# Optimization experiments

Hardware: AMD Instinct MI355X
Metric: run time of the kernel (lower is better)

## Reference

```python
import jax, jax.numpy as jnp
import numpy as np

D_MODEL = 1024
ED = 2048        # d_inner = expand_factor * d_model
N = 16           # d_state
DT_RANK = 64     # ceil(d_model/16)
K = 4            # d_conv
B_SZ = 4
L = 512


def _causal_depthwise_conv(u, w, b):
    # u: [B, L, ED], w: [ED, 1, K], b: [ED]
    xc = jnp.transpose(u, (0, 2, 1))  # [B, ED, L]
    xc = jax.lax.conv_general_dilated(
        xc, w, window_strides=(1,), padding=[(K - 1, 0)],
        feature_group_count=ED, dimension_numbers=('NCH', 'OIH', 'NCH'))
    xc = xc + b[None, :, None]
    return jnp.transpose(xc, (0, 2, 1))  # [B, L, ED]


def _ssm_branch(xz_half, z, conv_w, conv_b, Wx, Wdt, b_dt, A_log, Dp):
    # xz_half, z: [B, L, ED]
    x = jax.nn.silu(_causal_depthwise_conv(xz_half, conv_w, conv_b))
    dbc = x @ Wx.T  # [B, L, dt_rank + 2N]
    delta = dbc[..., :DT_RANK]
    Bm = dbc[..., DT_RANK:DT_RANK + N]
    Cm = dbc[..., DT_RANK + N:]
    delta = jax.nn.softplus(delta @ Wdt.T + b_dt)  # [B, L, ED]
    A = -jnp.exp(A_log)  # [ED, N]
    dA = jnp.exp(delta[..., None] * A)                        # [B, L, ED, N]
    bx = (delta[..., None] * Bm[:, :, None, :]) * x[..., None]  # [B, L, ED, N]
    dA_t = jnp.transpose(dA, (1, 0, 2, 3))
    bx_t = jnp.transpose(bx, (1, 0, 2, 3))
    c_t = jnp.transpose(Cm, (1, 0, 2))  # [L, B, N]
    h0 = jnp.zeros((x.shape[0], ED, N), dtype=x.dtype)

    def step(h, inp):
        dAi, bxi, ci = inp
        h = dAi * h + bxi
        return h, jnp.einsum('ben,bn->be', h, ci)

    _, ys = jax.lax.scan(step, h0, (dA_t, bx_t, c_t))
    y = jnp.transpose(ys, (1, 0, 2)) + Dp * x  # D skip connection
    return y * jax.nn.silu(z)                  # gate


def _mamba_block(x, W_in, conv_w, conv_b, Wx, Wdt, b_dt, A_log, Dp,
                 conv_w_b, conv_b_b, Wx_b, Wdt_b, b_dt_b, A_log_b, Dp_b, W_out):
    xz = x @ W_in.T  # [B, L, 2*ED]
    xf, zf = xz[..., :ED], xz[..., ED:]
    y = _ssm_branch(xf, zf, conv_w, conv_b, Wx, Wdt, b_dt, A_log, Dp)
    xz_r = xz[:, ::-1, :]
    xb, zb = xz_r[..., :ED], xz_r[..., ED:]
    y_b = _ssm_branch(xb, zb, conv_w_b, conv_b_b, Wx_b, Wdt_b, b_dt_b, A_log_b, Dp_b)
    y = (y + y_b[:, ::-1, :]) * 0.5
    return y @ W_out.T


def setup_inputs() -> dict:
    key = jax.random.key(0)
    ks = jax.random.split(key, 20)
    s = lambda k, shp, sc: jax.random.normal(k, shp, dtype=jnp.float32) * sc
    dt = jnp.exp(jax.random.uniform(ks[15], (ED,)) * (np.log(0.1) - np.log(0.001)) + np.log(0.001))
    dt = jnp.clip(dt, 1e-4, None)
    inv_dt = dt + jnp.log(-jnp.expm1(-dt))
    A_init = jnp.log(jnp.tile(jnp.arange(1, N + 1, dtype=jnp.float32), (ED, 1)))
    return {
        'x': s(ks[0], (B_SZ, L, D_MODEL), 1.0),
        'W_in': s(ks[1], (2 * ED, D_MODEL), D_MODEL ** -0.5),
        'conv_w': s(ks[2], (ED, 1, K), K ** -0.5),
        'conv_b': s(ks[3], (ED,), 0.02),
        'Wx': s(ks[4], (DT_RANK + 2 * N, ED), ED ** -0.5),
        'Wdt': jax.random.uniform(ks[5], (ED, DT_RANK), minval=-DT_RANK ** -0.5, maxval=DT_RANK ** -0.5),
        'b_dt': inv_dt,
        'A_log': A_init,
        'Dp': jnp.ones((ED,), dtype=jnp.float32),
        'conv_w_b': s(ks[6], (ED, 1, K), K ** -0.5),
        'conv_b_b': s(ks[7], (ED,), 0.02),
        'Wx_b': s(ks[8], (DT_RANK + 2 * N, ED), ED ** -0.5),
        'Wdt_b': jax.random.uniform(ks[9], (ED, DT_RANK), minval=-DT_RANK ** -0.5, maxval=DT_RANK ** -0.5),
        'b_dt_b': inv_dt,
        'A_log_b': A_init,
        'Dp_b': jnp.ones((ED,), dtype=jnp.float32),
        'W_out': s(ks[10], (D_MODEL, ED), ED ** -0.5),
    }


def reference(x, W_in, conv_w, conv_b, Wx, Wdt, b_dt, A_log, Dp,
              conv_w_b, conv_b_b, Wx_b, Wdt_b, b_dt_b, A_log_b, Dp_b, W_out):
    return _mamba_block(x, W_in, conv_w, conv_b, Wx, Wdt, b_dt, A_log, Dp,
                        conv_w_b, conv_b_b, Wx_b, Wdt_b, b_dt_b, A_log_b, Dp_b, W_out)
```

## Files before the change

### kernel.cpp

```cpp
#include <hip/hip_runtime.h>
#include <hip/hip_bf16.h>
#include <stdint.h>

typedef unsigned short ushort_t;
typedef __attribute__((ext_vector_type(8))) short short8;
typedef __attribute__((ext_vector_type(4))) float f32x4;
typedef __attribute__((ext_vector_type(2))) float f32x2;

__device__ __forceinline__ float b2f(ushort_t u) {
    union { uint32_t i; float f; } v; v.i = ((uint32_t)u) << 16; return v.f;
}
__device__ __forceinline__ ushort_t f2b(float f) {
    union { float f; uint32_t i; } v; v.f = f;
    uint32_t r = v.i + 0x7fff + ((v.i >> 16) & 1);
    return (ushort_t)(r >> 16);
}

#if __has_builtin(__builtin_amdgcn_exp2f)
#define EXP2(x) __builtin_amdgcn_exp2f(x)
#else
#define EXP2(x) __expf((x) * 0.69314718056f)
#endif

__device__ __forceinline__ void ll16(const ushort_t* g, ushort_t* l) {
    __builtin_amdgcn_global_load_lds(
        (const __attribute__((address_space(1))) uint32_t*)g,
        (__attribute__((address_space(3))) uint32_t*)l, 16, 0, 0);
}

template <int CTRL>
__device__ __forceinline__ float dpp_add(float p) {
    int v = __builtin_amdgcn_update_dpp(0, __float_as_int(p), CTRL, 0xF, 0xF, true);
    return p + __int_as_float(v);
}
#define DPP_XOR1 0xB1
#define DPP_XOR2 0x4E
#define DPP_HMIR 0x141

__device__ __forceinline__ void epi_wave_f32(
    float* sw, const f32x4* accg, float* dst0, int ldc, int lane)
{
    const int quad = lane >> 4, lr = lane & 15;
#pragma unroll
    for (int j = 0; j < 4; j++)
#pragma unroll
        for (int r = 0; r < 4; r++)
            sw[(quad * 4 + r) * 64 + j * 16 + lr] = accg[j][r];
    __asm__ volatile("s_waitcnt lgkmcnt(0)" ::: "memory");
#pragma unroll
    for (int t = 0; t < 4; t++) {
        int row = t * 4 + quad;
        float4 v = *(const float4*)(&sw[row * 64 + lr * 4]);
        *(float4*)(dst0 + (size_t)row * ldc + lr * 4) = v;
    }
}

__device__ __forceinline__ void epi_wave_b16(
    float* sw, const f32x4* accg, ushort_t* dst0, int ldc, int lane)
{
    const int quad = lane >> 4, lr = lane & 15;
#pragma unroll
    for (int j = 0; j < 4; j++)
#pragma unroll
        for (int r = 0; r < 4; r++)
            sw[(quad * 4 + r) * 64 + j * 16 + lr] = accg[j][r];
    __asm__ volatile("s_waitcnt lgkmcnt(0)" ::: "memory");
#pragma unroll
    for (int t = 0; t < 4; t++) {
        int row = t * 4 + quad;
        float4 v = *(const float4*)(&sw[row * 64 + lr * 4]);
        ushort4 o; o.x = f2b(v.x); o.y = f2b(v.y); o.z = f2b(v.z); o.w = f2b(v.w);
        *(ushort4*)(dst0 + (size_t)row * ldc + lr * 4) = o;
    }
}

struct CastSeg { const float4* src; ushort4* dst; };
struct CastArgs { CastSeg seg[7]; int start[8]; };

__global__ __launch_bounds__(256) void cast_multi(CastArgs a)
{
    int g = blockIdx.x * 256 + threadIdx.x;
    if (g >= a.start[7]) return;
    int s = 0;
#pragma unroll
    for (int i = 1; i < 7; i++) s += (g >= a.start[i]);
    int i = g - a.start[s];
    float4 v = a.seg[s].src[i];
    ushort4 o;
    o.x = f2b(v.x); o.y = f2b(v.y); o.z = f2b(v.z); o.w = f2b(v.w);
    a.seg[s].dst[i] = o;
}

#define BK 32

__global__ __launch_bounds__(256) void gemm_g1(
    const ushort_t* __restrict__ A, int lda,
    const ushort_t* __restrict__ B, int ldb,
    ushort_t* __restrict__ Cout, int ldc, int Kd)
{
    __shared__ ushort_t As[2][128 * BK];
    __shared__ ushort_t Bs[2][128 * BK];
    __shared__ float sepi[4][1024];

    const int tid  = threadIdx.x;
    const int m0   = blockIdx.y * 128;
    const int n0   = blockIdx.x * 128;
    const int wv   = tid >> 6;
    const int lane = tid & 63;
    const int wm   = (wv >> 1) * 64;
    const int wn   = (wv & 1) * 64;
    const int lr   = lane & 15;
    const int quad = lane >> 4;

    f32x4 acc[4][4];
#pragma unroll
    for (int i = 0; i < 4; i++)
#pragma unroll
        for (int j = 0; j < 4; j++) acc[i][j] = f32x4{0.f, 0.f, 0.f, 0.f};

    const int srA = wv * 32 + (lane >> 2);
    const int scA = (lane & 3) * 8;

    auto stage = [&](int bf_, int k0) {
        ll16(A + (size_t)(m0 + srA) * lda + k0 + scA,      &As[bf_][wv * 1024]);
        ll16(A + (size_t)(m0 + srA + 16) * lda + k0 + scA, &As[bf_][wv * 1024 + 512]);
        ll16(B + (size_t)(n0 + srA) * ldb + k0 + scA,      &Bs[bf_][wv * 1024]);
        ll16(B + (size_t)(n0 + srA + 16) * ldb + k0 + scA, &Bs[bf_][wv * 1024 + 512]);
    };

    const int nk = Kd / BK;
    stage(0, 0);
    __syncthreads();

    for (int t = 0; t < nk; ++t) {
        const int buf = t & 1;
        if (t + 1 < nk) stage(buf ^ 1, (t + 1) * BK);

        short8 af[4], bfr[4];
#pragma unroll
        for (int i = 0; i < 4; i++)
            af[i] = *(const short8*)(&As[buf][(wm + i * 16 + lr) * BK + quad * 8]);
#pragma unroll
        for (int j = 0; j < 4; j++)
            bfr[j] = *(const short8*)(&Bs[buf][(wn + j * 16 + lr) * BK + quad * 8]);
#pragma unroll
        for (int i = 0; i < 4; i++)
#pragma unroll
            for (int j = 0; j < 4; j++)
                acc[i][j] = __builtin_amdgcn_mfma_f32_16x16x32_bf16(af[i], bfr[j], acc[i][j], 0, 0, 0);
        __syncthreads();
    }

#pragma unroll
    for (int g = 0; g < 4; g++)
        epi_wave_b16(sepi[wv], acc[g],
                     Cout + (size_t)(m0 + wm + g * 16) * ldc + n0 + wn, ldc, lane);
}

__global__ __launch_bounds__(256) void gemm_g4(
    const ushort_t* __restrict__ A, int lda,
    const ushort_t* __restrict__ B, int ldb,
    float* __restrict__ Cout, int ldc, int Kd)
{
    __shared__ ushort_t As[2][64 * BK];
    __shared__ ushort_t Bs[2][128 * BK];
    __shared__ float sepi[4][1024];

    const int tid  = threadIdx.x;
    const int m0   = blockIdx.y * 64;
    const int n0   = blockIdx.x * 128;
    const int wv   = tid >> 6;
    const int lane = tid & 63;
    const int wm   = (wv >> 1) * 32;
    const int wn   = (wv & 1) * 64;
    const int lr   = lane & 15;
    const int quad = lane >> 4;

    f32x4 acc[2][4];
#pragma unroll
    for (int i = 0; i < 2; i++)
#pragma unroll
        for (int j = 0; j < 4; j++) acc[i][j] = f32x4{0.f, 0.f, 0.f, 0.f};

    const int srA = wv * 16 + (lane >> 2);
    const int srB = wv * 32 + (lane >> 2);
    const int sc  = (lane & 3) * 8;

    auto stage = [&](int bf_, int k0) {
        ll16(A + (size_t)(m0 + srA) * lda + k0 + sc,      &As[bf_][wv * 512]);
        ll16(B + (size_t)(n0 + srB) * ldb + k0 + sc,      &Bs[bf_][wv * 1024]);
        ll16(B + (size_t)(n0 + srB + 16) * ldb + k0 + sc, &Bs[bf_][wv * 1024 + 512]);
    };

    const int nk = Kd / BK;
    stage(0, 0);
    __syncthreads();

    for (int t = 0; t < nk; ++t) {
        const int buf = t & 1;
        if (t + 1 < nk) stage(buf ^ 1, (t + 1) * BK);

        short8 af[2], bfr[4];
#pragma unroll
        for (int i = 0; i < 2; i++)
            af[i] = *(const short8*)(&As[buf][(wm + i * 16 + lr) * BK + quad * 8]);
#pragma unroll
        for (int j = 0; j < 4; j++)
            bfr[j] = *(const short8*)(&Bs[buf][(wn + j * 16 + lr) * BK + quad * 8]);
#pragma unroll
        for (int i = 0; i < 2; i++)
#pragma unroll
            for (int j = 0; j < 4; j++)
                acc[i][j] = __builtin_amdgcn_mfma_f32_16x16x32_bf16(af[i], bfr[j], acc[i][j], 0, 0, 0);
        __syncthreads();
    }

#pragma unroll
    for (int g = 0; g < 2; g++)
        epi_wave_f32(sepi[wv], acc[g],
                     Cout + (size_t)(m0 + wm + g * 16) * ldc + n0 + wn, ldc, lane);
}

__global__ __launch_bounds__(256) void gemm_g2(
    const ushort_t* __restrict__ xc, const ushort_t* __restrict__ wx,
    float* __restrict__ part)
{
    __shared__ ushort_t As[2][128 * BK];
    __shared__ ushort_t Bs[2][128 * BK];
    __shared__ float sepi[4][1024];

    const int sk = blockIdx.x, mb = blockIdx.y, br = blockIdx.z;
    const ushort_t* A = xc + (size_t)br * 2048 * 2048;
    const ushort_t* B = wx + (size_t)br * 96 * 2048;
    float* C = part + (size_t)(sk * 2 + br) * 2048 * 96;
    const int m0 = mb * 128;
    const int kb = sk * 256;

    const int tid  = threadIdx.x;
    const int wv   = tid >> 6;
    const int lane = tid & 63;
    const int wm   = (wv >> 1) * 64;
    const int wn   = (wv & 1) * 64;
    const int lr   = lane & 15;
    const int quad = lane >> 4;

    f32x4 acc[4][4];
#pragma unroll
    for (int i = 0; i < 4; i++)
#pragma unroll
        for (int j = 0; j < 4; j++) acc[i][j] = f32x4{0.f, 0.f, 0.f, 0.f};

    const int srA = wv * 32 + (lane >> 2);
    const int sc  = (lane & 3) * 8;

    auto stage = [&](int bf_, int k0) {
        ll16(A + (size_t)(m0 + srA) * 2048 + k0 + sc,      &As[bf_][wv * 1024]);
        ll16(A + (size_t)(m0 + srA + 16) * 2048 + k0 + sc, &As[bf_][wv * 1024 + 512]);
        ll16(B + (size_t)(srA) * 2048 + k0 + sc,           &Bs[bf_][wv * 1024]);
        ll16(B + (size_t)(srA + 16) * 2048 + k0 + sc,      &Bs[bf_][wv * 1024 + 512]);
    };

    stage(0, kb);
    __syncthreads();

    for (int t = 0; t < 8; ++t) {
        const int buf = t & 1;
        if (t + 1 < 8) stage(buf ^ 1, kb + (t + 1) * BK);

        short8 af[4], bfr[4];
#pragma unroll
        for (int i = 0; i < 4; i++)
            af[i] = *(const short8*)(&As[buf][(wm + i * 16 + lr) * BK + quad * 8]);
#pragma unroll
        for (int j = 0; j < 4; j++)
            bfr[j] = *(const short8*)(&Bs[buf][(wn + j * 16 + lr) * BK + quad * 8]);
#pragma unroll
        for (int i = 0; i < 4; i++)
#pragma unroll
            for (int j = 0; j < 4; j++)
                acc[i][j] = __builtin_amdgcn_mfma_f32_16x16x32_bf16(af[i], bfr[j], acc[i][j], 0, 0, 0);
        __syncthreads();
    }

    float* sw = sepi[wv];
#pragma unroll
    for (int g = 0; g < 4; g++) {
#pragma unroll
        for (int j = 0; j < 4; j++)
#pragma unroll
            for (int r = 0; r < 4; r++)
                sw[(quad * 4 + r) * 64 + j * 16 + lr] = acc[g][j][r];
        __asm__ volatile("s_waitcnt lgkmcnt(0)" ::: "memory");
        int col = wn + lr * 4;
#pragma unroll
        for (int t = 0; t < 4; t++) {
            int row = t * 4 + quad;
            if (col < 96) {
                float4 v = *(const float4*)(&sw[row * 64 + lr * 4]);
                *(float4*)(C + (size_t)(m0 + wm + g * 16 + row) * 96 + col) = v;
            }
        }
    }
}

__global__ __launch_bounds__(256) void reduce_dbc(
    const float4* __restrict__ part, ushort4* __restrict__ dbc16)
{
    int g = blockIdx.x * 256 + threadIdx.x;
    const int S = 2 * 2048 * 96 / 4;
    float4 r = part[g];
#pragma unroll
    for (int i = 1; i < 8; i++) {
        float4 p = part[g + i * S];
        r.x += p.x; r.y += p.y; r.z += p.z; r.w += p.w;
    }
    ushort4 o; o.x = f2b(r.x); o.y = f2b(r.y); o.z = f2b(r.z); o.w = f2b(r.w);
    dbc16[g] = o;
}

__global__ __launch_bounds__(256) void gemm_g3(
    const ushort_t* __restrict__ dbc16, const ushort_t* __restrict__ wdt,
    ushort_t* __restrict__ delta,
    const float* __restrict__ bdt_f, const float* __restrict__ bdt_b)
{
    __shared__ ushort_t As[2][128 * BK];
    __shared__ ushort_t Bs[2][128 * BK];
    __shared__ float sepi[4][1024];

    const int br = blockIdx.z;
    const ushort_t* A = dbc16 + (size_t)br * 2048 * 96;
    const ushort_t* B = wdt + (size_t)br * 2048 * 64;
    ushort_t* C = delta + (size_t)br * 2048 * 2048;
    const float* bias = br ? bdt_b : bdt_f;

    const int tid  = threadIdx.x;
    const int m0   = blockIdx.y * 128;
    const int n0   = blockIdx.x * 128;
    const int wv   = tid >> 6;
    const int lane = tid & 63;
    const int wm   = (wv >> 1) * 64;
    const int wn   = (wv & 1) * 64;
    const int lr   = lane & 15;
    const int quad = lane >> 4;

    f32x4 acc[4][4];
#pragma unroll
    for (int i = 0; i < 4; i++)
#pragma unroll
        for (int j = 0; j < 4; j++) acc[i][j] = f32x4{0.f, 0.f, 0.f, 0.f};

    const int srA = wv * 32 + (lane >> 2);
    const int sc  = (lane & 3) * 8;

    auto stage = [&](int bf_, int k0) {
        ll16(A + (size_t)(m0 + srA) * 96 + k0 + sc,       &As[bf_][wv * 1024]);
        ll16(A + (size_t)(m0 + srA + 16) * 96 + k0 + sc,  &As[bf_][wv * 1024 + 512]);
        ll16(B + (size_t)(n0 + srA) * 64 + k0 + sc,       &Bs[bf_][wv * 1024]);
        ll16(B + (size_t)(n0 + srA + 16) * 64 + k0 + sc,  &Bs[bf_][wv * 1024 + 512]);
    };

    stage(0, 0);
    __syncthreads();

    for (int t = 0; t < 2; ++t) {
        const int buf = t & 1;
        if (t + 1 < 2) stage(buf ^ 1, (t + 1) * BK);

        short8 af[4], bfr[4];
#pragma unroll
        for (int i = 0; i < 4; i++)
            af[i] = *(const short8*)(&As[buf][(wm + i * 16 + lr) * BK + quad * 8]);
#pragma unroll
        for (int j = 0; j < 4; j++)
            bfr[j] = *(const short8*)(&Bs[buf][(wn + j * 16 + lr) * BK + quad * 8]);
#pragma unroll
        for (int i = 0; i < 4; i++)
#pragma unroll
            for (int j = 0; j < 4; j++)
                acc[i][j] = __builtin_amdgcn_mfma_f32_16x16x32_bf16(af[i], bfr[j], acc[i][j], 0, 0, 0);
        __syncthreads();
    }

    float bn[4];
#pragma unroll
    for (int j = 0; j < 4; j++) bn[j] = bias[n0 + wn + j * 16 + lr];
#pragma unroll
    for (int g = 0; g < 4; g++)
#pragma unroll
        for (int j = 0; j < 4; j++)
#pragma unroll
            for (int r = 0; r < 4; r++) {
                float x = acc[g][j][r] + bn[j];
                float sp = fmaxf(x, 0.f) + __logf(1.f + __expf(-fabsf(x)));
                acc[g][j][r] = sp;
            }

#pragma unroll
    for (int g = 0; g < 4; g++)
        epi_wave_b16(sepi[wv], acc[g],
                     C + (size_t)(m0 + wm + g * 16) * 2048 + n0 + wn, 2048, lane);
}

__global__ __launch_bounds__(256) void conv_silu_kernel(
    const ushort_t* __restrict__ xz,
    const float* __restrict__ w_f, const float* __restrict__ cb_f,
    const float* __restrict__ w_b, const float* __restrict__ cb_b,
    ushort_t* __restrict__ xc16)
{
    int g = blockIdx.x * 256 + threadIdx.x;
    int e  = g & 2047;
    int t  = (g >> 11) & 511;
    int b  = (g >> 20) & 3;
    int br = g >> 22;

    const float* w  = br ? w_b  : w_f;
    const float* cb = br ? cb_b : cb_f;

    float acc = cb[e];
    float4 wv = *(const float4*)(w + e * 4);
    float wk[4] = { wv.x, wv.y, wv.z, wv.w };

#pragma unroll
    for (int k = 0; k < 4; k++) {
        int tp = t - 3 + k;
        if (tp >= 0) {
            int row = br ? (511 - tp) : tp;
            acc += wk[k] * b2f(xz[((size_t)(b * 512 + row)) * 4096 + e]);
        }
    }
    float s = acc / (1.f + __expf(-acc));
    xc16[g] = f2b(s);
}

__global__ __launch_bounds__(256, 4) void scan_kernel(
    const ushort_t* __restrict__ delta,
    const ushort_t* __restrict__ xc,
    const ushort_t* __restrict__ dbc16,
    const ushort_t* __restrict__ xz,
    const float* __restrict__ Alog_f, const float* __restrict__ Alog_b,
    const float* __restrict__ Dp_f,   const float* __restrict__ Dp_b,
    ushort_t* __restrict__ yf, ushort_t* __restrict__ yb)
{
    const int blk = blockIdx.x;
    const int eg = blk & 63;
    const int b  = (blk >> 6) & 3;
    const int br = blk >> 8;
    const int e0 = eg * 32;

    const int tid = threadIdx.x;
    const int n2  = tid & 7;
    const int el  = tid >> 3;
    const int e   = e0 + el;

    const float* Alog = br ? Alog_b : Alog_f;
    const float* Dpp  = br ? Dp_b   : Dp_f;
    f32x2 a01;
    a01.x = -__expf(Alog[e * 16 + n2]) * 1.44269504f;
    a01.y = -__expf(Alog[e * 16 + n2 + 8]) * 1.44269504f;

    size_t tb = ((size_t)br * 4 + b) * 512;
    const ushort_t* dlt  = delta + tb * 2048;
    const ushort_t* xcb  = xc    + tb * 2048;
    const ushort_t* dbcb = dbc16 + tb * 96;
    ushort_t* y = (br ? yb : yf) + (size_t)b * 512 * 2048;

    __shared__ float sd [2][32][36];
    __shared__ float sdx[2][32][36];
    __shared__ float sBp[2][8][34][2];
    __shared__ float sCp[2][8][34][2];
    __shared__ float sy [2][32][33];

    const int stt = tid >> 3;
    const int seg = tid & 7;
    const int sg4 = seg * 4;
    const int sdk = (seg & 3) * 8;

    float4 rD = *(const float4*)(Dpp + e0 + sg4);

    uint2 rdx, rx, rbc, rz;
    uint2 rx_c, rx_f, rz_c, rz_f;

    auto load_regs = [&](int c) {
        int row = c * 32 + stt;
        rdx = *(const uint2*)(dlt + (size_t)row * 2048 + e0 + sg4);
        rx  = *(const uint2*)(xcb + (size_t)row * 2048 + e0 + sg4);
        rbc = *(const uint2*)(dbcb + (size_t)row * 96 + 64 + sg4);
        int orow = br ? (511 - row) : row;
        rz  = *(const uint2*)(xz + ((size_t)(b * 512 + orow)) * 4096 + 2048 + e0 + sg4);
    };
    auto write_lds = [&](int buf) {
        const uint32_t dw[2] = { rdx.x, rdx.y };
        const uint32_t xw[2] = { rx.x, rx.y };
        const int col = stt ^ sdk;
#pragma unroll
        for (int k = 0; k < 2; k++) {
            float d0 = b2f((ushort_t)(dw[k] & 0xffff));
            float d1 = b2f((ushort_t)(dw[k] >> 16));
            float x0 = b2f((ushort_t)(xw[k] & 0xffff));
            float x1 = b2f((ushort_t)(xw[k] >> 16));
            sd [buf][sg4 + 2 * k][col]     = d0;
            sd [buf][sg4 + 2 * k + 1][col] = d1;
            sdx[buf][sg4 + 2 * k][col]     = d0 * x0;
            sdx[buf][sg4 + 2 * k + 1][col] = d1 * x1;
        }
        float* arr = (seg < 4) ? &sBp[buf][0][0][0] : &sCp[buf][0][0][0];
        const int nb = (seg & 3) * 4;
        const uint32_t bw[2] = { rbc.x, rbc.y };
#pragma unroll
        for (int k = 0; k < 2; k++) {
            int na = nb + 2 * k, nbd = nb + 2 * k + 1;
            arr[(na  & 7) * 68 + stt * 2 + (na  >> 3)] = b2f((ushort_t)(bw[k] & 0xffff));
            arr[(nbd & 7) * 68 + stt * 2 + (nbd >> 3)] = b2f((ushort_t)(bw[k] >> 16));
        }
    };
    auto flush = [&](int cm1) {
        const int bufm1 = cm1 & 1;
        int row = cm1 * 32 + stt;
        const uint32_t zw[2] = { rz_f.x, rz_f.y };
        float zv[4];
#pragma unroll
        for (int k = 0; k < 2; k++) {
            zv[2 * k]     = b2f((ushort_t)(zw[k] & 0xffff));
            zv[2 * k + 1] = b2f((ushort_t)(zw[k] >> 16));
        }
        float pv[4];
#pragma unroll
        for (int k = 0; k < 4; k++) pv[k] = sy[bufm1][stt][sg4 + k];
        const uint32_t xw[2] = { rx_f.x, rx_f.y };
        float xvv[4];
#pragma unroll
        for (int k = 0; k < 2; k++) {
            xvv[2 * k]     = b2f((ushort_t)(xw[k] & 0xffff));
            xvv[2 * k + 1] = b2f((ushort_t)(xw[k] >> 16));
        }
        const float Dv[4] = { rD.x, rD.y, rD.z, rD.w };
        uint32_t op[2];
#pragma unroll
        for (int k = 0; k < 2; k++) {
            float ga = (pv[2 * k]     + Dv[2 * k]     * xvv[2 * k])     *
                       (zv[2 * k]     / (1.f + __expf(-zv[2 * k])));
            float gb = (pv[2 * k + 1] + Dv[2 * k + 1] * xvv[2 * k + 1]) *
                       (zv[2 * k + 1] / (1.f + __expf(-zv[2 * k + 1])));
            op[k] = (uint32_t)f2b(ga) | ((uint32_t)f2b(gb) << 16);
        }
        *(uint2*)(y + (size_t)row * 2048 + e0 + sg4) = make_uint2(op[0], op[1]);
    };

    f32x2 h01 = f32x2{0.f, 0.f};
    const int elk = ((el >> 2) & 3) * 8;

    load_regs(0);
    write_lds(0);
    rx_c = rx; rz_c = rz;

    for (int c = 0; c < 16; ++c) {
        if (c < 15) load_regs(c + 1);
        __syncthreads();
        const int buf = c & 1;

        auto LDQ = [&](int tq, f32x4& dv, f32x4& dxv, f32x4& bq0, f32x4& bq1,
                       f32x4& cq0, f32x4& cq1) {
            const int tc = tq ^ elk;
            dv  = *(const f32x4*)(&sd [buf][el][tc]);
            dxv = *(const f32x4*)(&sdx[buf][el][tc]);
            bq0 = *(const f32x4*)(&sBp[buf][n2][tq][0]);
            bq1 = *(const f32x4*)(&sBp[buf][n2][tq + 2][0]);
            cq0 = *(const f32x4*)(&sCp[buf][n2][tq][0]);
            cq1 = *(const f32x4*)(&sCp[buf][n2][tq + 2][0]);
        };

        f32x4 dv_p, dxv_p, bq0_p, bq1_p, cq0_p, cq1_p;
        LDQ(0, dv_p, dxv_p, bq0_p, bq1_p, cq0_p, cq1_p);

        float pout[4];
#pragma unroll 4
        for (int tq = 0; tq < 32; tq += 4) {
            const f32x4 dv = dv_p, dxv = dxv_p;
            const f32x4 bq0 = bq0_p, bq1 = bq1_p, cq0 = cq0_p, cq1 = cq1_p;
            LDQ((tq + 4) & 31, dv_p, dxv_p, bq0_p, bq1_p, cq0_p, cq1_p);

#define SSTEP(DC, DXC, BT, CT, TI)                                   \
            {                                                        \
                f32x2 arg = a01 * (DC);                              \
                f32x2 ee; ee.x = EXP2(arg.x); ee.y = EXP2(arg.y);    \
                h01 = ee * h01 + (BT) * (DXC);                       \
                f32x2 pp = h01 * (CT);                               \
                float p = pp.x + pp.y;                               \
                p = dpp_add<DPP_XOR1>(p);                            \
                p = dpp_add<DPP_XOR2>(p);                            \
                p = dpp_add<DPP_HMIR>(p);                            \
                pout[TI] = p;                                        \
            }
            SSTEP(dv.x, dxv.x, bq0.xy, cq0.xy, 0)
            SSTEP(dv.y, dxv.y, bq0.zw, cq0.zw, 1)
            SSTEP(dv.z, dxv.z, bq1.xy, cq1.xy, 2)
            SSTEP(dv.w, dxv.w, bq1.zw, cq1.zw, 3)
#undef SSTEP

            if (n2 == 0) {
                sy[buf][tq + 0][el] = pout[0];
                sy[buf][tq + 1][el] = pout[1];
                sy[buf][tq + 2][el] = pout[2];
                sy[buf][tq + 3][el] = pout[3];
            }
        }

        if (c > 0) flush(c - 1);

        if (c < 15) {
            write_lds((c + 1) & 1);
            rx_f = rx_c; rz_f = rz_c;
            rx_c = rx;   rz_c = rz;
        } else {
            rx_f = rx_c; rz_f = rz_c;
        }
    }
    __syncthreads();
    flush(15);
}

__global__ __launch_bounds__(256) void combine_kernel(
    const uint2* __restrict__ yf, const uint2* __restrict__ yb,
    uint2* __restrict__ yc)
{
    int g = blockIdx.x * 256 + threadIdx.x;
    int e4 = g & 511;
    int t  = (g >> 9) & 511;
    int b  = g >> 18;
    uint2 a = yf[g];
    uint2 c = yb[((size_t)(b * 512 + 511 - t)) * 512 + e4];
    uint2 o;
    o.x = (uint32_t)f2b(0.5f * (b2f((ushort_t)(a.x & 0xffff)) + b2f((ushort_t)(c.x & 0xffff)))) |
          ((uint32_t)f2b(0.5f * (b2f((ushort_t)(a.x >> 16)) + b2f((ushort_t)(c.x >> 16)))) << 16);
    o.y = (uint32_t)f2b(0.5f * (b2f((ushort_t)(a.y & 0xffff)) + b2f((ushort_t)(c.y & 0xffff)))) |
          ((uint32_t)f2b(0.5f * (b2f((ushort_t)(a.y >> 16)) + b2f((ushort_t)(c.y >> 16)))) << 16);
    yc[g] = o;
}

static const size_t TT = 2048;
static const size_t OFF_XZ16  = 0;
static const size_t OFF_XC16  = OFF_XZ16  + TT*4096*2;
static const size_t OFF_DBC16 = OFF_XC16  + 2*TT*2048*2;
static const size_t OFF_DELTA = OFF_DBC16 + 2*TT*96*2;
static const size_t OFF_YF    = OFF_DELTA + 2*TT*2048*2;
static const size_t OFF_YB    = OFF_YF    + TT*2048*2;
static const size_t OFF_YC16  = OFF_YB    + TT*2048*2;
static const size_t OFF_X16   = OFF_YC16  + TT*2048*2;
static const size_t OFF_WIN16 = OFF_X16   + TT*1024*2;
static const size_t OFF_WX16  = OFF_WIN16 + 4096*1024*2;
static const size_t OFF_WDT16 = OFF_WX16  + 2*96*2048*2;
static const size_t OFF_WOUT16= OFF_WDT16 + 2*2048*64*2;
static const size_t OFF_PART  = OFF_WOUT16+ 1024*2048*2;

extern "C" void kernel_launch(void* const* d_in, const int* in_sizes, int n_in,
                              void* d_out, int out_size, void* d_ws, size_t ws_size,
                              hipStream_t stream) {
    const float* x       = (const float*)d_in[0];
    const float* W_in    = (const float*)d_in[1];
    const float* conv_w  = (const float*)d_in[2];
    const float* conv_b  = (const float*)d_in[3];
    const float* Wx      = (const float*)d_in[4];
    const float* Wdt     = (const float*)d_in[5];
    const float* b_dt    = (const float*)d_in[6];
    const float* A_log   = (const float*)d_in[7];
    const float* Dp      = (const float*)d_in[8];
    const float* conv_w_b= (const float*)d_in[9];
    const float* conv_b_b= (const float*)d_in[10];
    const float* Wx_b    = (const float*)d_in[11];
    const float* Wdt_b   = (const float*)d_in[12];
    const float* b_dt_b  = (const float*)d_in[13];
    const float* A_log_b = (const float*)d_in[14];
    const float* Dp_b    = (const float*)d_in[15];
    const float* W_out   = (const float*)d_in[16];
    float* out = (float*)d_out;

    char* ws = (char*)d_ws;
    ushort_t* xz16  = (ushort_t*)(ws + OFF_XZ16);
    ushort_t* xc16  = (ushort_t*)(ws + OFF_XC16);
    ushort_t* dbc16 = (ushort_t*)(ws + OFF_DBC16);
    ushort_t* delta = (ushort_t*)(ws + OFF_DELTA);
    ushort_t* yf    = (ushort_t*)(ws + OFF_YF);
    ushort_t* yb    = (ushort_t*)(ws + OFF_YB);
    ushort_t* yc16  = (ushort_t*)(ws + OFF_YC16);
    ushort_t* x16   = (ushort_t*)(ws + OFF_X16);
    ushort_t* win16 = (ushort_t*)(ws + OFF_WIN16);
    ushort_t* wx16  = (ushort_t*)(ws + OFF_WX16);
    ushort_t* wdt16 = (ushort_t*)(ws + OFF_WDT16);
    ushort_t* wout16= (ushort_t*)(ws + OFF_WOUT16);
    float*    part  = (float*)(ws + OFF_PART);

    dim3 blk(256);

    CastArgs ca;
    const int n4s[7] = {524288, 1048576, 49152, 49152, 32768, 32768, 524288};
    ca.seg[0] = { (const float4*)x,     (ushort4*)x16 };
    ca.seg[1] = { (const float4*)W_in,  (ushort4*)win16 };
    ca.seg[2] = { (const float4*)Wx,    (ushort4*)wx16 };
    ca.seg[3] = { (const float4*)Wx_b,  (ushort4*)(wx16 + 96 * 2048) };
    ca.seg[4] = { (const float4*)Wdt,   (ushort4*)wdt16 };
    ca.seg[5] = { (const float4*)Wdt_b, (ushort4*)(wdt16 + 2048 * 64) };
    ca.seg[6] = { (const float4*)W_out, (ushort4*)wout16 };
    ca.start[0] = 0;
    for (int i = 0; i < 7; i++) ca.start[i + 1] = ca.start[i] + n4s[i];
    cast_multi<<<(ca.start[7] + 255) / 256, blk, 0, stream>>>(ca);

    gemm_g1<<<dim3(32, 16), blk, 0, stream>>>(x16, 1024, win16, 1024, xz16, 4096, 1024);

    conv_silu_kernel<<<32768, blk, 0, stream>>>(xz16, conv_w, conv_b, conv_w_b, conv_b_b, xc16);

    gemm_g2<<<dim3(8, 16, 2), blk, 0, stream>>>(xc16, wx16, part);
    reduce_dbc<<<384, blk, 0, stream>>>((const float4*)part, (ushort4*)dbc16);

    gemm_g3<<<dim3(16, 16, 2), blk, 0, stream>>>(dbc16, wdt16, delta, b_dt, b_dt_b);

    scan_kernel<<<512, blk, 0, stream>>>(delta, xc16, dbc16, xz16, A_log, A_log_b, Dp, Dp_b, yf, yb);

    combine_kernel<<<4096, blk, 0, stream>>>((const uint2*)yf, (const uint2*)yb, (uint2*)yc16);

    gemm_g4<<<dim3(8, 32), blk, 0, stream>>>(yc16, 2048, wout16, 2048, out, 1024, 2048);
}
```

Baseline: 271.2 us.

## Fuse forward/backward combine into output GEMM A-load and split K in two

The separate combine kernel is removed. The output GEMM now loads the forward and time-reversed backward scan outputs directly, averages them in registers and writes the bf16 result into shared memory. The output GEMM is also split along K into two halves over a z grid dimension, writing fp32 partials into the no-longer-needed delta buffer, and a new reduce kernel sums them. This removes one launch and the round trip through the combined bf16 tensor, and doubles the block count for better CU occupancy. In exchange it adds a partial-sum write/read pass and a register-staged A path instead of the direct load-to-LDS helper.

```diff
diff --git a/kernel.cpp b/kernel.cpp
--- a/kernel.cpp
+++ b/kernel.cpp
@@ -158,9 +158,9 @@
 }
 
 __global__ __launch_bounds__(256) void gemm_g4(
-    const ushort_t* __restrict__ A, int lda,
+    const ushort_t* __restrict__ yfp, const ushort_t* __restrict__ ybp,
     const ushort_t* __restrict__ B, int ldb,
-    float* __restrict__ Cout, int ldc, int Kd)
+    float* __restrict__ part)
 {
     __shared__ ushort_t As[2][64 * BK];
     __shared__ ushort_t Bs[2][128 * BK];
@@ -169,6 +169,8 @@
     const int tid  = threadIdx.x;
     const int m0   = blockIdx.y * 64;
     const int n0   = blockIdx.x * 128;
+    const int kz   = blockIdx.z;
+    const int kbase = kz * 1024;
     const int wv   = tid >> 6;
     const int lane = tid & 63;
     const int wm   = (wv >> 1) * 32;
@@ -186,19 +188,49 @@
     const int srB = wv * 32 + (lane >> 2);
     const int sc  = (lane & 3) * 8;
 
-    auto stage = [&](int bf_, int k0) {
-        ll16(A + (size_t)(m0 + srA) * lda + k0 + sc,      &As[bf_][wv * 512]);
-        ll16(B + (size_t)(n0 + srB) * ldb + k0 + sc,      &Bs[bf_][wv * 1024]);
-        ll16(B + (size_t)(n0 + srB + 16) * ldb + k0 + sc, &Bs[bf_][wv * 1024 + 512]);
-    };
-
-    const int nk = Kd / BK;
-    stage(0, 0);
+    const int arow = m0 + srA;
+    const int t_   = arow & 511;
+    const size_t yf_off = (size_t)arow * 2048;
+    const size_t yb_off = (size_t)(arow - t_ + 511 - t_) * 2048;
+
+    uint4 ra, rb;
+    auto loadA = [&](int k0) {
+        ra = *(const uint4*)(yfp + yf_off + kbase + k0 + sc);
+        rb = *(const uint4*)(ybp + yb_off + kbase + k0 + sc);
+    };
+    auto writeA = [&](int bf_) {
+        const uint32_t pa[4] = { ra.x, ra.y, ra.z, ra.w };
+        const uint32_t pb[4] = { rb.x, rb.y, rb.z, rb.w };
+        uint32_t w[4];
+#pragma unroll
+        for (int k = 0; k < 4; k++) {
+            float a0 = b2f((ushort_t)(pa[k] & 0xffff));
+            float a1 = b2f((ushort_t)(pa[k] >> 16));
+            float c0 = b2f((ushort_t)(pb[k] & 0xffff));
+            float c1 = b2f((ushort_t)(pb[k] >> 16));
+            w[k] = (uint32_t)f2b(0.5f * (a0 + c0)) |
+                   ((uint32_t)f2b(0.5f * (a1 + c1)) << 16);
+        }
+        *(uint4*)(&As[bf_][wv * 512 + (lane >> 2) * 32 + (lane & 3) * 8]) =
+            make_uint4(w[0], w[1], w[2], w[3]);
+    };
+    auto stageB = [&](int bf_, int k0) {
+        ll16(B + (size_t)(n0 + srB) * ldb + kbase + k0 + sc,      &Bs[bf_][wv * 1024]);
+        ll16(B + (size_t)(n0 + srB + 16) * ldb + kbase + k0 + sc, &Bs[bf_][wv * 1024 + 512]);
+    };
+
+    const int nk = 1024 / BK;
+    loadA(0);
+    stageB(0, 0);
+    writeA(0);
     __syncthreads();
 
     for (int t = 0; t < nk; ++t) {
         const int buf = t & 1;
-        if (t + 1 < nk) stage(buf ^ 1, (t + 1) * BK);
+        if (t + 1 < nk) {
+            loadA((t + 1) * BK);
+            stageB(buf ^ 1, (t + 1) * BK);
+        }
 
         short8 af[2], bfr[4];
 #pragma unroll
@@ -212,13 +244,26 @@
 #pragma unroll
             for (int j = 0; j < 4; j++)
                 acc[i][j] = __builtin_amdgcn_mfma_f32_16x16x32_bf16(af[i], bfr[j], acc[i][j], 0, 0, 0);
+
+        if (t + 1 < nk) writeA(buf ^ 1);
         __syncthreads();
     }
 
+    float* Cout = part + (size_t)kz * 2048 * 1024;
 #pragma unroll
     for (int g = 0; g < 2; g++)
         epi_wave_f32(sepi[wv], acc[g],
-                     Cout + (size_t)(m0 + wm + g * 16) * ldc + n0 + wn, ldc, lane);
+                     Cout + (size_t)(m0 + wm + g * 16) * 1024 + n0 + wn, 1024, lane);
+}
+
+__global__ __launch_bounds__(256) void reduce_g4(
+    const float4* __restrict__ part, float4* __restrict__ out)
+{
+    int g = blockIdx.x * 256 + threadIdx.x;
+    const int S = 2048 * 1024 / 4;
+    float4 a = part[g], b = part[g + S];
+    float4 o; o.x = a.x + b.x; o.y = a.y + b.y; o.z = a.z + b.z; o.w = a.w + b.w;
+    out[g] = o;
 }
 
 __global__ __launch_bounds__(256) void gemm_g2(
@@ -617,24 +662,6 @@
     }
     __syncthreads();
     flush(15);
-}
-
-__global__ __launch_bounds__(256) void combine_kernel(
-    const uint2* __restrict__ yf, const uint2* __restrict__ yb,
-    uint2* __restrict__ yc)
-{
-    int g = blockIdx.x * 256 + threadIdx.x;
-    int e4 = g & 511;
-    int t  = (g >> 9) & 511;
-    int b  = g >> 18;
-    uint2 a = yf[g];
-    uint2 c = yb[((size_t)(b * 512 + 511 - t)) * 512 + e4];
-    uint2 o;
-    o.x = (uint32_t)f2b(0.5f * (b2f((ushort_t)(a.x & 0xffff)) + b2f((ushort_t)(c.x & 0xffff)))) |
-          ((uint32_t)f2b(0.5f * (b2f((ushort_t)(a.x >> 16)) + b2f((ushort_t)(c.x >> 16)))) << 16);
-    o.y = (uint32_t)f2b(0.5f * (b2f((ushort_t)(a.y & 0xffff)) + b2f((ushort_t)(c.y & 0xffff)))) |
-          ((uint32_t)f2b(0.5f * (b2f((ushort_t)(a.y >> 16)) + b2f((ushort_t)(c.y >> 16)))) << 16);
-    yc[g] = o;
 }
 
 static const size_t TT = 2048;
@@ -681,13 +708,13 @@
     ushort_t* delta = (ushort_t*)(ws + OFF_DELTA);
     ushort_t* yf    = (ushort_t*)(ws + OFF_YF);
     ushort_t* yb    = (ushort_t*)(ws + OFF_YB);
-    ushort_t* yc16  = (ushort_t*)(ws + OFF_YC16);
     ushort_t* x16   = (ushort_t*)(ws + OFF_X16);
     ushort_t* win16 = (ushort_t*)(ws + OFF_WIN16);
     ushort_t* wx16  = (ushort_t*)(ws + OFF_WX16);
     ushort_t* wdt16 = (ushort_t*)(ws + OFF_WDT16);
     ushort_t* wout16= (ushort_t*)(ws + OFF_WOUT16);
     float*    part  = (float*)(ws + OFF_PART);
+    float*    part4 = (float*)(ws + OFF_DELTA);
 
     dim3 blk(256);
 
@@ -715,7 +742,6 @@
 
     scan_kernel<<<512, blk, 0, stream>>>(delta, xc16, dbc16, xz16, A_log, A_log_b, Dp, Dp_b, yf, yb);
 
-    combine_kernel<<<4096, blk, 0, stream>>>((const uint2*)yf, (const uint2*)yb, (uint2*)yc16);
-
-    gemm_g4<<<dim3(8, 32), blk, 0, stream>>>(yc16, 2048, wout16, 2048, out, 1024, 2048);
-}
+    gemm_g4<<<dim3(8, 32, 2), blk, 0, stream>>>(yf, yb, wout16, 2048, part4);
+    reduce_g4<<<2048, blk, 0, stream>>>((const float4*)part4, (float4*)out);
+}
```

Result: no change. 266.6 us (-1.7%).
